# Optimization experiments

Hardware: AMD Instinct MI355X
Metric: run time of the kernel (lower is better)

Reference implementation:

```python
import jax, jax.numpy as jnp
import numpy as np

N, E, F, H = 100000, 1000000, 128, 64
BN_EPS = 1e-3  # keras BatchNormalization default epsilon


def setup_inputs() -> dict:
    key = jax.random.key(0)
    k_x, k_src, k_dst, k_w = jax.random.split(key, 4)
    node_features = jax.random.normal(k_x, (N, F), dtype=jnp.float32)
    # Ensure every node appears at least once as a source so that
    # deg**-0.5 is finite (the original code implicitly assumes this).
    src = jnp.concatenate([
        jnp.arange(N, dtype=jnp.int32),
        jax.random.randint(k_src, (E - N,), 0, N, dtype=jnp.int32),
    ])
    dst = jax.random.randint(k_dst, (E,), 0, N, dtype=jnp.int32)
    edge_index = jnp.stack([src, dst], axis=1)  # [E, 2]
    # glorot_uniform for kernel
    limit = np.sqrt(6.0 / (F + H)).astype(np.float32)
    W = jax.random.uniform(k_w, (F, H), dtype=jnp.float32, minval=-limit, maxval=limit)
    b = jnp.zeros((H,), dtype=jnp.float32)
    bn_gamma = jnp.ones((H,), dtype=jnp.float32)
    bn_beta = jnp.zeros((H,), dtype=jnp.float32)
    bn_mean = jnp.zeros((H,), dtype=jnp.float32)
    bn_var = jnp.ones((H,), dtype=jnp.float32)
    return dict(node_features=node_features, W=W, b=b, bn_gamma=bn_gamma,
                bn_beta=bn_beta, bn_mean=bn_mean, bn_var=bn_var,
                edge_index=edge_index)


def reference(node_features, W, b, bn_gamma, bn_beta, bn_mean, bn_var, edge_index):
    n = node_features.shape[0]
    src = edge_index[:, 0]
    dst = edge_index[:, 1]
    # Dense transform; dropout is identity in inference (training=False).
    h = node_features @ W + b  # [N, H]
    # Out-degree per node (segments keyed by src, matching the TF code).
    deg = jax.ops.segment_sum(jnp.ones(src.shape, h.dtype), src, num_segments=n)  # [N]
    inv_sqrt_deg = deg ** -0.5
    # Per-edge symmetric-style scaling: deg(src)^-0.5 * deg(dst)^-0.5 * h[dst]
    edge_scale = inv_sqrt_deg[src] * inv_sqrt_deg[dst]  # [E]
    neigh = edge_scale[:, None] * h[dst]  # [E, H]
    agg = 0.5 * jax.ops.segment_sum(neigh, src, num_segments=n)  # [N, H]
    # Self term: segment_mean of deg(src) * h[src] over src segments.
    self_term = deg[src][:, None] * h[src]  # [E, H]
    self_sum = jax.ops.segment_sum(self_term, src, num_segments=n)  # [N, H]
    self_mean = self_sum / jnp.maximum(deg, 1.0)[:, None]
    agg = agg + 0.5 * self_mean
    # BatchNormalization in inference mode.
    out = (agg - bn_mean) * (bn_gamma * jax.lax.rsqrt(bn_var + BN_EPS)) + bn_beta
    return out
```

## Files before the change

kernel.cpp:

```cpp
#include <hip/hip_runtime.h>

#define BN_EPS 0.001f
#define CAP 32

typedef __attribute__((ext_vector_type(8))) short bf16x8;
typedef __attribute__((ext_vector_type(4))) float f32x4;

__device__ __forceinline__ unsigned short f2bf(float f) {
  unsigned u = __float_as_uint(f);
  u += 0x7fffu + ((u >> 16) & 1u);
  return (unsigned short)(u >> 16);
}
__device__ __forceinline__ unsigned scale2(unsigned u, float s) {
  float lo = __uint_as_float(u << 16) * s;
  float hi = __uint_as_float(u & 0xffff0000u) * s;
  return (((unsigned)f2bf(hi)) << 16) | (unsigned)f2bf(lo);
}

__global__ __launch_bounds__(256) void k_fused(
    const float* __restrict__ X, const float* __restrict__ W,
    const float* __restrict__ B, unsigned short* __restrict__ hb, int N, int Gg,
    const int2* __restrict__ ei, int* __restrict__ cnt,
    int* __restrict__ ell_t, int E, int Gs) {
  __shared__ float WtF[4096];

  int g = blockIdx.x / 7;
  int r = blockIdx.x % 7;
  int tid = threadIdx.x;

  if (r >= 2) {
    int chunk = g * 5 + (r - 2);
    if (chunk >= Gs) return;
    int e = chunk * 256 + tid;
    if (e < E) {
      int2 sd = ei[e];
      int pos = atomicAdd(&cnt[sd.x], 1);
      if (pos < CAP) ell_t[(size_t)pos * N + sd.x] = sd.y;
    }
    return;
  }

  int tile = g * 2 + r;
  if (tile >= Gg) return;

  char* Wt = (char*)WtF;
  const float4* W4 = (const float4*)W;
  for (int i = tid; i < 2048; i += 256) {
    float4 v = W4[i];
    int k = i >> 4;
    int col0 = (i & 15) << 2;
    int kb2 = k << 1;
    *(unsigned short*)(Wt + (((col0 + 0) << 8) | (kb2 ^ (((col0 + 0) & 7) << 4)))) = f2bf(v.x);
    *(unsigned short*)(Wt + (((col0 + 1) << 8) | (kb2 ^ (((col0 + 1) & 7) << 4)))) = f2bf(v.y);
    *(unsigned short*)(Wt + (((col0 + 2) << 8) | (kb2 ^ (((col0 + 2) & 7) << 4)))) = f2bf(v.z);
    *(unsigned short*)(Wt + (((col0 + 3) << 8) | (kb2 ^ (((col0 + 3) & 7) << 4)))) = f2bf(v.w);
  }
  __syncthreads();

  int lane = tid & 63;
  int w = tid >> 6;
  int l15 = lane & 15;
  int lk = lane >> 4;

  int row0 = tile * 64;
  int rA = row0 + w * 16 + l15;
  bool rowok = rA < N;
  const float* xp = X + (size_t)rA * 128 + (lk << 3);

  f32x4 acc[4];
  #pragma unroll
  for (int n = 0; n < 4; ++n) {
    float bv = B[(n << 4) + l15];
    acc[n] = (f32x4){bv, bv, bv, bv};
  }

  #pragma unroll
  for (int kb = 0; kb < 4; ++kb) {
    bf16x8 af = {0, 0, 0, 0, 0, 0, 0, 0};
    if (rowok) {
      float4 x0 = *(const float4*)(xp + kb * 32);
      float4 x1 = *(const float4*)(xp + kb * 32 + 4);
      af[0] = (short)f2bf(x0.x); af[1] = (short)f2bf(x0.y);
      af[2] = (short)f2bf(x0.z); af[3] = (short)f2bf(x0.w);
      af[4] = (short)f2bf(x1.x); af[5] = (short)f2bf(x1.y);
      af[6] = (short)f2bf(x1.z); af[7] = (short)f2bf(x1.w);
    }
    int kbyte = (kb << 6) | (lk << 4);
    #pragma unroll
    for (int n = 0; n < 4; ++n) {
      int col = (n << 4) + l15;
      bf16x8 bfr = *(const bf16x8*)(Wt + ((col << 8) | (kbyte ^ ((col & 7) << 4))));
      acc[n] = __builtin_amdgcn_mfma_f32_16x16x32_bf16(af, bfr, acc[n], 0, 0, 0);
    }
  }

  int rbase = row0 + w * 16 + (lk << 2);
  #pragma unroll
  for (int n = 0; n < 4; ++n) {
    #pragma unroll
    for (int q = 0; q < 4; ++q) {
      int row = rbase + q;
      if (row < N) hb[(size_t)row * 64 + (n << 4) + l15] = f2bf(acc[n][q]);
    }
  }
}

__global__ __launch_bounds__(256) void k_scale(const unsigned int* __restrict__ hb32,
                                               const int* __restrict__ cnt,
                                               unsigned int* __restrict__ hbs32, int N) {
  int t = blockIdx.x * 256 + threadIdx.x;
  int node = t >> 3;
  int q = t & 7;
  if (node >= N) return;
  int c = cnt[node];
  float s = rsqrtf((float)((c > 0) ? c : 1));
  uint4 v = ((const uint4*)(hb32 + (size_t)node * 32))[q];
  v.x = scale2(v.x, s); v.y = scale2(v.y, s);
  v.z = scale2(v.z, s); v.w = scale2(v.w, s);
  ((uint4*)(hbs32 + (size_t)node * 32))[q] = v;
}

__global__ __launch_bounds__(256) void k_agg2(const int* __restrict__ cnt,
                                              const int* __restrict__ ell_t,
                                              const unsigned int* __restrict__ hb32,
                                              const unsigned int* __restrict__ hbs32,
                                              const float* __restrict__ gamma,
                                              const float* __restrict__ beta,
                                              const float* __restrict__ mean,
                                              const float* __restrict__ var,
                                              float* __restrict__ out, int N) {
  __shared__ int lds_dst[CAP * 64];
  __shared__ int lds_cnt[64];

  int tid = threadIdx.x;
  int node0 = blockIdx.x * 64;

  if (tid < 64) {
    int n = node0 + tid;
    lds_cnt[tid] = (n < N) ? cnt[n] : 0;
  }
  for (int i = tid; i < CAP * 64; i += 256) {
    int j = i & 63;
    int p = i >> 6;
    int n = node0 + j;
    lds_dst[i] = (n < N) ? ell_t[(size_t)p * N + n] : 0;
  }
  __syncthreads();

  int hw = tid >> 5;
  int fp = tid & 31;

  float2 gm = *(const float2*)&gamma[fp * 2];
  float2 bt = *(const float2*)&beta[fp * 2];
  float2 mn = *(const float2*)&mean[fp * 2];
  float2 vr = *(const float2*)&var[fp * 2];
  float gsx = gm.x * rsqrtf(vr.x + BN_EPS);
  float gsy = gm.y * rsqrtf(vr.y + BN_EPS);

  #pragma unroll
  for (int t = 0; t < 8; ++t) {
    int j = hw * 8 + t;
    int node = node0 + j;
    if (node >= N) continue;
    int c0 = lds_cnt[j];
    int c = (c0 < CAP) ? c0 : CAP;
    unsigned us = hb32[(size_t)node * 32 + fp];

    float ax = 0.f, ay = 0.f;
    int q = 0;
    for (; q + 8 <= c; q += 8) {
      int d[8];
      #pragma unroll
      for (int i = 0; i < 8; ++i) {
        int dr = lds_dst[(q + i) * 64 + j];
        d[i] = ((unsigned)dr < (unsigned)N) ? dr : 0;
      }
      unsigned u[8];
      #pragma unroll
      for (int i = 0; i < 8; ++i) u[i] = hbs32[(size_t)d[i] * 32 + fp];
      #pragma unroll
      for (int i = 0; i < 8; ++i) {
        ax += __uint_as_float(u[i] << 16);
        ay += __uint_as_float(u[i] & 0xffff0000u);
      }
    }
    if (q + 4 <= c) {
      int d0 = lds_dst[(q + 0) * 64 + j]; d0 = ((unsigned)d0 < (unsigned)N) ? d0 : 0;
      int d1 = lds_dst[(q + 1) * 64 + j]; d1 = ((unsigned)d1 < (unsigned)N) ? d1 : 0;
      int d2 = lds_dst[(q + 2) * 64 + j]; d2 = ((unsigned)d2 < (unsigned)N) ? d2 : 0;
      int d3 = lds_dst[(q + 3) * 64 + j]; d3 = ((unsigned)d3 < (unsigned)N) ? d3 : 0;
      unsigned u0 = hbs32[(size_t)d0 * 32 + fp];
      unsigned u1 = hbs32[(size_t)d1 * 32 + fp];
      unsigned u2 = hbs32[(size_t)d2 * 32 + fp];
      unsigned u3 = hbs32[(size_t)d3 * 32 + fp];
      ax += __uint_as_float(u0 << 16);
      ay += __uint_as_float(u0 & 0xffff0000u);
      ax += __uint_as_float(u1 << 16);
      ay += __uint_as_float(u1 & 0xffff0000u);
      ax += __uint_as_float(u2 << 16);
      ay += __uint_as_float(u2 & 0xffff0000u);
      ax += __uint_as_float(u3 << 16);
      ay += __uint_as_float(u3 & 0xffff0000u);
      q += 4;
    }
    for (; q < c; ++q) {
      int dq = lds_dst[q * 64 + j];
      dq = ((unsigned)dq < (unsigned)N) ? dq : 0;
      unsigned u = hbs32[(size_t)dq * 32 + fp];
      ax += __uint_as_float(u << 16);
      ay += __uint_as_float(u & 0xffff0000u);
    }

    float hx = __uint_as_float(us << 16);
    float hy = __uint_as_float(us & 0xffff0000u);
    float degf = (float)c0;
    float isd_n = rsqrtf((float)((c0 > 0) ? c0 : 1));
    float rx = 0.5f * (isd_n * ax + degf * hx);
    float ry = 0.5f * (isd_n * ay + degf * hy);

    float2 o;
    o.x = (rx - mn.x) * gsx + bt.x;
    o.y = (ry - mn.y) * gsy + bt.y;
    *(float2*)&out[(size_t)node * 64 + fp * 2] = o;
  }
}

__global__ __launch_bounds__(256) void k_agg2_g(const int* __restrict__ cnt,
                                                const int* __restrict__ ell_t,
                                                const unsigned int* __restrict__ hb32,
                                                const float* __restrict__ gamma,
                                                const float* __restrict__ beta,
                                                const float* __restrict__ mean,
                                                const float* __restrict__ var,
                                                float* __restrict__ out, int N) {
  __shared__ int lds_dst[CAP * 64];
  __shared__ int lds_cnt[64];

  int tid = threadIdx.x;
  int node0 = blockIdx.x * 64;

  if (tid < 64) {
    int n = node0 + tid;
    lds_cnt[tid] = (n < N) ? cnt[n] : 0;
  }
  for (int i = tid; i < CAP * 64; i += 256) {
    int j = i & 63;
    int p = i >> 6;
    int n = node0 + j;
    lds_dst[i] = (n < N) ? ell_t[(size_t)p * N + n] : 0;
  }
  __syncthreads();

  int hw = tid >> 5;
  int fp = tid & 31;

  float2 gm = *(const float2*)&gamma[fp * 2];
  float2 bt = *(const float2*)&beta[fp * 2];
  float2 mn = *(const float2*)&mean[fp * 2];
  float2 vr = *(const float2*)&var[fp * 2];
  float gsx = gm.x * rsqrtf(vr.x + BN_EPS);
  float gsy = gm.y * rsqrtf(vr.y + BN_EPS);

  for (int t = 0; t < 8; ++t) {
    int j = hw * 8 + t;
    int node = node0 + j;
    if (node >= N) continue;
    int c0 = lds_cnt[j];
    int c = (c0 < CAP) ? c0 : CAP;
    unsigned us = hb32[(size_t)node * 32 + fp];

    float ax = 0.f, ay = 0.f;
    int q = 0;
    for (; q + 4 <= c; q += 4) {
      int d0 = lds_dst[(q + 0) * 64 + j]; d0 = ((unsigned)d0 < (unsigned)N) ? d0 : 0;
      int d1 = lds_dst[(q + 1) * 64 + j]; d1 = ((unsigned)d1 < (unsigned)N) ? d1 : 0;
      int d2 = lds_dst[(q + 2) * 64 + j]; d2 = ((unsigned)d2 < (unsigned)N) ? d2 : 0;
      int d3 = lds_dst[(q + 3) * 64 + j]; d3 = ((unsigned)d3 < (unsigned)N) ? d3 : 0;
      float s0 = rsqrtf((float)max(cnt[d0], 1));
      float s1 = rsqrtf((float)max(cnt[d1], 1));
      float s2 = rsqrtf((float)max(cnt[d2], 1));
      float s3 = rsqrtf((float)max(cnt[d3], 1));
      unsigned u0 = hb32[(size_t)d0 * 32 + fp];
      unsigned u1 = hb32[(size_t)d1 * 32 + fp];
      unsigned u2 = hb32[(size_t)d2 * 32 + fp];
      unsigned u3 = hb32[(size_t)d3 * 32 + fp];
      ax = fmaf(s0, __uint_as_float(u0 << 16), ax);
      ay = fmaf(s0, __uint_as_float(u0 & 0xffff0000u), ay);
      ax = fmaf(s1, __uint_as_float(u1 << 16), ax);
      ay = fmaf(s1, __uint_as_float(u1 & 0xffff0000u), ay);
      ax = fmaf(s2, __uint_as_float(u2 << 16), ax);
      ay = fmaf(s2, __uint_as_float(u2 & 0xffff0000u), ay);
      ax = fmaf(s3, __uint_as_float(u3 << 16), ax);
      ay = fmaf(s3, __uint_as_float(u3 & 0xffff0000u), ay);
    }
    for (; q < c; ++q) {
      int dq = lds_dst[q * 64 + j];
      dq = ((unsigned)dq < (unsigned)N) ? dq : 0;
      float sq = rsqrtf((float)max(cnt[dq], 1));
      unsigned u = hb32[(size_t)dq * 32 + fp];
      ax = fmaf(sq, __uint_as_float(u << 16), ax);
      ay = fmaf(sq, __uint_as_float(u & 0xffff0000u), ay);
    }

    float hx = __uint_as_float(us << 16);
    float hy = __uint_as_float(us & 0xffff0000u);
    float degf = (float)c0;
    float isd_n = rsqrtf((float)((c0 > 0) ? c0 : 1));
    float rx = 0.5f * (isd_n * ax + degf * hx);
    float ry = 0.5f * (isd_n * ay + degf * hy);

    float2 o;
    o.x = (rx - mn.x) * gsx + bt.x;
    o.y = (ry - mn.y) * gsy + bt.y;
    *(float2*)&out[(size_t)node * 64 + fp * 2] = o;
  }
}

extern "C" void kernel_launch(void* const* d_in, const int* in_sizes, int n_in,
                              void* d_out, int out_size, void* d_ws, size_t ws_size,
                              hipStream_t stream) {
  const float* X     = (const float*)d_in[0];
  const float* W     = (const float*)d_in[1];
  const float* B     = (const float*)d_in[2];
  const float* gamma = (const float*)d_in[3];
  const float* beta  = (const float*)d_in[4];
  const float* mean  = (const float*)d_in[5];
  const float* var   = (const float*)d_in[6];
  const int2*  ei    = (const int2*)d_in[7];

  int N = in_sizes[0] / 128;
  int E = in_sizes[7] / 2;
  float* out = (float*)d_out;

  size_t hb_elems = (size_t)N * 64;
  size_t need_hbs = hb_elems * 2 * 2 + (size_t)N * CAP * 4 + (size_t)N * 4;

  int Gs = (E + 255) / 256;
  int Gg = (N + 63) / 64;
  int g7 = (Gg + 1) / 2;
  int g5 = (Gs + 4) / 5;
  int groups = (g7 > g5) ? g7 : g5;
  int Ga = (N + 63) / 64;

  if (ws_size >= need_hbs) {
    unsigned short* hb  = (unsigned short*)d_ws;
    unsigned short* hbs = hb + hb_elems;
    int*            ell = (int*)(hbs + hb_elems);
    int*            cnt = ell + (size_t)N * CAP;

    hipMemsetAsync(cnt, 0, (size_t)N * sizeof(int), stream);
    k_fused<<<groups * 7, 256, 0, stream>>>(X, W, B, hb, N, Gg, ei, cnt, ell, E, Gs);
    k_scale<<<(N * 8 + 255) / 256, 256, 0, stream>>>((const unsigned int*)hb, cnt,
                                                     (unsigned int*)hbs, N);
    k_agg2<<<Ga, 256, 0, stream>>>(cnt, ell, (const unsigned int*)hb,
                                   (const unsigned int*)hbs,
                                   gamma, beta, mean, var, out, N);
  } else {
    unsigned short* hb  = (unsigned short*)d_ws;
    int*            ell = (int*)(hb + hb_elems);
    int*            cnt = ell + (size_t)N * CAP;

    hipMemsetAsync(cnt, 0, (size_t)N * sizeof(int), stream);
    k_fused<<<groups * 7, 256, 0, stream>>>(X, W, B, hb, N, Gg, ei, cnt, ell, E, Gs);
    k_agg2_g<<<Ga, 256, 0, stream>>>(cnt, ell, (const unsigned int*)hb,
                                     gamma, beta, mean, var, out, N);
  }
}
```

Baseline: 199.5 us.

## Fuse all stages into one persistent cooperative kernel with grid syncs

Replaces the memset plus three kernel launches with a single cooperative persistent kernel that zeroes counts, runs the GEMM and the ELL build, scales h, and aggregates, separated by grid-wide syncs. The aim is to remove launch gaps and the per-launch tail effects between the small stages. In exchange it limits the grid to resident blocks, loops over tiles, and adds grid-barrier cost plus the W-to-LDS conversion once per block. It also drops the 4-wide remainder block in the old k_agg2 fallback.

```diff
diff --git a/kernel.cpp b/kernel.cpp
--- a/kernel.cpp
+++ b/kernel.cpp
@@ -1,4 +1,7 @@
 #include <hip/hip_runtime.h>
+#include <hip/hip_cooperative_groups.h>
+
+namespace cg = cooperative_groups;
 
 #define BN_EPS 0.001f
 #define CAP 32
@@ -15,6 +18,259 @@
   float lo = __uint_as_float(u << 16) * s;
   float hi = __uint_as_float(u & 0xffff0000u) * s;
   return (((unsigned)f2bf(hi)) << 16) | (unsigned)f2bf(lo);
+}
+
+__global__ __launch_bounds__(256, 4) void k_all(
+    const float* __restrict__ X, const float* __restrict__ W,
+    const float* __restrict__ B, const float* __restrict__ gamma,
+    const float* __restrict__ beta, const float* __restrict__ mean,
+    const float* __restrict__ var, const int2* __restrict__ ei,
+    unsigned short* __restrict__ hb, unsigned short* __restrict__ hbs,
+    int* __restrict__ ell_t, int* __restrict__ cnt,
+    float* __restrict__ out, int N, int E, int use_hbs) {
+  __shared__ float WtF[4096];
+  cg::grid_group gg = cg::this_grid();
+  int tid = threadIdx.x;
+  int bid = blockIdx.x;
+  int nb  = gridDim.x;
+
+  for (int i = bid * 256 + tid; i < N; i += nb * 256) cnt[i] = 0;
+  gg.sync();
+
+  char* Wt = (char*)WtF;
+  {
+    const float4* W4 = (const float4*)W;
+    for (int i = tid; i < 2048; i += 256) {
+      float4 v = W4[i];
+      int k = i >> 4;
+      int col0 = (i & 15) << 2;
+      int kb2 = k << 1;
+      *(unsigned short*)(Wt + (((col0 + 0) << 8) | (kb2 ^ (((col0 + 0) & 7) << 4)))) = f2bf(v.x);
+      *(unsigned short*)(Wt + (((col0 + 1) << 8) | (kb2 ^ (((col0 + 1) & 7) << 4)))) = f2bf(v.y);
+      *(unsigned short*)(Wt + (((col0 + 2) << 8) | (kb2 ^ (((col0 + 2) & 7) << 4)))) = f2bf(v.z);
+      *(unsigned short*)(Wt + (((col0 + 3) << 8) | (kb2 ^ (((col0 + 3) & 7) << 4)))) = f2bf(v.w);
+    }
+  }
+  __syncthreads();
+
+  int Gg = (N + 63) >> 6;
+  int Gs = (E + 255) >> 8;
+  int g7 = (Gg + 1) >> 1;
+  int g5 = (Gs + 4) / 5;
+  int groups = (g7 > g5) ? g7 : g5;
+  int total = groups * 7;
+
+  int lane = tid & 63;
+  int w = tid >> 6;
+  int l15 = lane & 15;
+  int lk = lane >> 4;
+
+  for (int u = bid; u < total; u += nb) {
+    int g = u / 7, r = u % 7;
+    if (r >= 2) {
+      int chunk = g * 5 + (r - 2);
+      if (chunk < Gs) {
+        int e = chunk * 256 + tid;
+        if (e < E) {
+          int2 sd = ei[e];
+          int pos = atomicAdd(&cnt[sd.x], 1);
+          if (pos < CAP) ell_t[(size_t)pos * N + sd.x] = sd.y;
+        }
+      }
+    } else {
+      int tile = g * 2 + r;
+      if (tile < Gg) {
+        int row0 = tile * 64;
+        int rA = row0 + w * 16 + l15;
+        bool rowok = rA < N;
+        const float* xp = X + (size_t)rA * 128 + (lk << 3);
+
+        f32x4 acc[4];
+        #pragma unroll
+        for (int n = 0; n < 4; ++n) {
+          float bv = B[(n << 4) + l15];
+          acc[n] = (f32x4){bv, bv, bv, bv};
+        }
+        #pragma unroll
+        for (int kb = 0; kb < 4; ++kb) {
+          bf16x8 af = {0, 0, 0, 0, 0, 0, 0, 0};
+          if (rowok) {
+            float4 x0 = *(const float4*)(xp + kb * 32);
+            float4 x1 = *(const float4*)(xp + kb * 32 + 4);
+            af[0] = (short)f2bf(x0.x); af[1] = (short)f2bf(x0.y);
+            af[2] = (short)f2bf(x0.z); af[3] = (short)f2bf(x0.w);
+            af[4] = (short)f2bf(x1.x); af[5] = (short)f2bf(x1.y);
+            af[6] = (short)f2bf(x1.z); af[7] = (short)f2bf(x1.w);
+          }
+          int kbyte = (kb << 6) | (lk << 4);
+          #pragma unroll
+          for (int n = 0; n < 4; ++n) {
+            int col = (n << 4) + l15;
+            bf16x8 bfr = *(const bf16x8*)(Wt + ((col << 8) | (kbyte ^ ((col & 7) << 4))));
+            acc[n] = __builtin_amdgcn_mfma_f32_16x16x32_bf16(af, bfr, acc[n], 0, 0, 0);
+          }
+        }
+        int rbase = row0 + w * 16 + (lk << 2);
+        #pragma unroll
+        for (int n = 0; n < 4; ++n) {
+          #pragma unroll
+          for (int q = 0; q < 4; ++q) {
+            int row = rbase + q;
+            if (row < N) hb[(size_t)row * 64 + (n << 4) + l15] = f2bf(acc[n][q]);
+          }
+        }
+      }
+    }
+  }
+  __threadfence();
+  gg.sync();
+
+  if (use_hbs) {
+    const unsigned* hb32r = (const unsigned*)hb;
+    unsigned* hbs32w = (unsigned*)hbs;
+    int tot = N * 8;
+    for (int t = bid * 256 + tid; t < tot; t += nb * 256) {
+      int node = t >> 3;
+      int q = t & 7;
+      int c = cnt[node];
+      float s = rsqrtf((float)((c > 0) ? c : 1));
+      uint4 v = ((const uint4*)(hb32r + (size_t)node * 32))[q];
+      v.x = scale2(v.x, s); v.y = scale2(v.y, s);
+      v.z = scale2(v.z, s); v.w = scale2(v.w, s);
+      ((uint4*)(hbs32w + (size_t)node * 32))[q] = v;
+    }
+  }
+  __threadfence();
+  gg.sync();
+
+  int* lds_dst = (int*)WtF;
+  int* lds_cnt = ((int*)WtF) + CAP * 64;
+  const unsigned* hb32 = (const unsigned*)hb;
+  const unsigned* hbs32 = (const unsigned*)hbs;
+  int hw = tid >> 5;
+  int fp = tid & 31;
+
+  float2 gm = *(const float2*)&gamma[fp * 2];
+  float2 bt = *(const float2*)&beta[fp * 2];
+  float2 mn = *(const float2*)&mean[fp * 2];
+  float2 vr = *(const float2*)&var[fp * 2];
+  float gsx = gm.x * rsqrtf(vr.x + BN_EPS);
+  float gsy = gm.y * rsqrtf(vr.y + BN_EPS);
+
+  int Ga = (N + 63) >> 6;
+  for (int tile = bid; tile < Ga; tile += nb) {
+    int node0 = tile << 6;
+    if (tid < 64) {
+      int n = node0 + tid;
+      lds_cnt[tid] = (n < N) ? cnt[n] : 0;
+    }
+    for (int i = tid; i < CAP * 64; i += 256) {
+      int j = i & 63;
+      int p = i >> 6;
+      int n = node0 + j;
+      lds_dst[i] = (n < N) ? ell_t[(size_t)p * N + n] : 0;
+    }
+    __syncthreads();
+
+    #pragma unroll 2
+    for (int t = 0; t < 8; ++t) {
+      int j = hw * 8 + t;
+      int node = node0 + j;
+      if (node < N) {
+        int c0 = lds_cnt[j];
+        int c = (c0 < CAP) ? c0 : CAP;
+        unsigned us = hb32[(size_t)node * 32 + fp];
+
+        float ax = 0.f, ay = 0.f;
+        if (use_hbs) {
+          int q = 0;
+          for (; q + 8 <= c; q += 8) {
+            int d[8];
+            #pragma unroll
+            for (int i = 0; i < 8; ++i) {
+              int dr = lds_dst[(q + i) * 64 + j];
+              d[i] = ((unsigned)dr < (unsigned)N) ? dr : 0;
+            }
+            unsigned u[8];
+            #pragma unroll
+            for (int i = 0; i < 8; ++i) u[i] = hbs32[(size_t)d[i] * 32 + fp];
+            #pragma unroll
+            for (int i = 0; i < 8; ++i) {
+              ax += __uint_as_float(u[i] << 16);
+              ay += __uint_as_float(u[i] & 0xffff0000u);
+            }
+          }
+          if (q + 4 <= c) {
+            int d0 = lds_dst[(q + 0) * 64 + j]; d0 = ((unsigned)d0 < (unsigned)N) ? d0 : 0;
+            int d1 = lds_dst[(q + 1) * 64 + j]; d1 = ((unsigned)d1 < (unsigned)N) ? d1 : 0;
+            int d2 = lds_dst[(q + 2) * 64 + j]; d2 = ((unsigned)d2 < (unsigned)N) ? d2 : 0;
+            int d3 = lds_dst[(q + 3) * 64 + j]; d3 = ((unsigned)d3 < (unsigned)N) ? d3 : 0;
+            unsigned u0 = hbs32[(size_t)d0 * 32 + fp];
+            unsigned u1 = hbs32[(size_t)d1 * 32 + fp];
+            unsigned u2 = hbs32[(size_t)d2 * 32 + fp];
+            unsigned u3 = hbs32[(size_t)d3 * 32 + fp];
+            ax += __uint_as_float(u0 << 16); ay += __uint_as_float(u0 & 0xffff0000u);
+            ax += __uint_as_float(u1 << 16); ay += __uint_as_float(u1 & 0xffff0000u);
+            ax += __uint_as_float(u2 << 16); ay += __uint_as_float(u2 & 0xffff0000u);
+            ax += __uint_as_float(u3 << 16); ay += __uint_as_float(u3 & 0xffff0000u);
+            q += 4;
+          }
+          for (; q < c; ++q) {
+            int dq = lds_dst[q * 64 + j];
+            dq = ((unsigned)dq < (unsigned)N) ? dq : 0;
+            unsigned u = hbs32[(size_t)dq * 32 + fp];
+            ax += __uint_as_float(u << 16);
+            ay += __uint_as_float(u & 0xffff0000u);
+          }
+        } else {
+          int q = 0;
+          for (; q + 4 <= c; q += 4) {
+            int d0 = lds_dst[(q + 0) * 64 + j]; d0 = ((unsigned)d0 < (unsigned)N) ? d0 : 0;
+            int d1 = lds_dst[(q + 1) * 64 + j]; d1 = ((unsigned)d1 < (unsigned)N) ? d1 : 0;
+            int d2 = lds_dst[(q + 2) * 64 + j]; d2 = ((unsigned)d2 < (unsigned)N) ? d2 : 0;
+            int d3 = lds_dst[(q + 3) * 64 + j]; d3 = ((unsigned)d3 < (unsigned)N) ? d3 : 0;
+            float s0 = rsqrtf((float)max(cnt[d0], 1));
+            float s1 = rsqrtf((float)max(cnt[d1], 1));
+            float s2 = rsqrtf((float)max(cnt[d2], 1));
+            float s3 = rsqrtf((float)max(cnt[d3], 1));
+            unsigned u0 = hb32[(size_t)d0 * 32 + fp];
+            unsigned u1 = hb32[(size_t)d1 * 32 + fp];
+            unsigned u2 = hb32[(size_t)d2 * 32 + fp];
+            unsigned u3 = hb32[(size_t)d3 * 32 + fp];
+            ax = fmaf(s0, __uint_as_float(u0 << 16), ax);
+            ay = fmaf(s0, __uint_as_float(u0 & 0xffff0000u), ay);
+            ax = fmaf(s1, __uint_as_float(u1 << 16), ax);
+            ay = fmaf(s1, __uint_as_float(u1 & 0xffff0000u), ay);
+            ax = fmaf(s2, __uint_as_float(u2 << 16), ax);
+            ay = fmaf(s2, __uint_as_float(u2 & 0xffff0000u), ay);
+            ax = fmaf(s3, __uint_as_float(u3 << 16), ax);
+            ay = fmaf(s3, __uint_as_float(u3 & 0xffff0000u), ay);
+          }
+          for (; q < c; ++q) {
+            int dq = lds_dst[q * 64 + j];
+            dq = ((unsigned)dq < (unsigned)N) ? dq : 0;
+            float sq = rsqrtf((float)max(cnt[dq], 1));
+            unsigned u = hb32[(size_t)dq * 32 + fp];
+            ax = fmaf(sq, __uint_as_float(u << 16), ax);
+            ay = fmaf(sq, __uint_as_float(u & 0xffff0000u), ay);
+          }
+        }
+
+        float hx = __uint_as_float(us << 16);
+        float hy = __uint_as_float(us & 0xffff0000u);
+        float degf = (float)c0;
+        float isd_n = rsqrtf((float)((c0 > 0) ? c0 : 1));
+        float rx = 0.5f * (isd_n * ax + degf * hx);
+        float ry = 0.5f * (isd_n * ay + degf * hy);
+
+        float2 o;
+        o.x = (rx - mn.x) * gsx + bt.x;
+        o.y = (ry - mn.y) * gsy + bt.y;
+        *(float2*)&out[(size_t)node * 64 + fp * 2] = o;
+      }
+    }
+    __syncthreads();
+  }
 }
 
 __global__ __launch_bounds__(256) void k_fused(
@@ -23,7 +279,6 @@
     const int2* __restrict__ ei, int* __restrict__ cnt,
     int* __restrict__ ell_t, int E, int Gs) {
   __shared__ float WtF[4096];
-
   int g = blockIdx.x / 7;
   int r = blockIdx.x % 7;
   int tid = threadIdx.x;
@@ -73,7 +328,6 @@
     float bv = B[(n << 4) + l15];
     acc[n] = (f32x4){bv, bv, bv, bv};
   }
-
   #pragma unroll
   for (int kb = 0; kb < 4; ++kb) {
     bf16x8 af = {0, 0, 0, 0, 0, 0, 0, 0};
@@ -93,7 +347,6 @@
       acc[n] = __builtin_amdgcn_mfma_f32_16x16x32_bf16(af, bfr, acc[n], 0, 0, 0);
     }
   }
-
   int rbase = row0 + w * 16 + (lk << 2);
   #pragma unroll
   for (int n = 0; n < 4; ++n) {
@@ -131,7 +384,6 @@
                                               float* __restrict__ out, int N) {
   __shared__ int lds_dst[CAP * 64];
   __shared__ int lds_cnt[64];
-
   int tid = threadIdx.x;
   int node0 = blockIdx.x * 64;
 
@@ -149,7 +401,6 @@
 
   int hw = tid >> 5;
   int fp = tid & 31;
-
   float2 gm = *(const float2*)&gamma[fp * 2];
   float2 bt = *(const float2*)&beta[fp * 2];
   float2 mn = *(const float2*)&mean[fp * 2];
@@ -184,25 +435,6 @@
         ay += __uint_as_float(u[i] & 0xffff0000u);
       }
     }
-    if (q + 4 <= c) {
-      int d0 = lds_dst[(q + 0) * 64 + j]; d0 = ((unsigned)d0 < (unsigned)N) ? d0 : 0;
-      int d1 = lds_dst[(q + 1) * 64 + j]; d1 = ((unsigned)d1 < (unsigned)N) ? d1 : 0;
-      int d2 = lds_dst[(q + 2) * 64 + j]; d2 = ((unsigned)d2 < (unsigned)N) ? d2 : 0;
-      int d3 = lds_dst[(q + 3) * 64 + j]; d3 = ((unsigned)d3 < (unsigned)N) ? d3 : 0;
-      unsigned u0 = hbs32[(size_t)d0 * 32 + fp];
-      unsigned u1 = hbs32[(size_t)d1 * 32 + fp];
-      unsigned u2 = hbs32[(size_t)d2 * 32 + fp];
-      unsigned u3 = hbs32[(size_t)d3 * 32 + fp];
-      ax += __uint_as_float(u0 << 16);
-      ay += __uint_as_float(u0 & 0xffff0000u);
-      ax += __uint_as_float(u1 << 16);
-      ay += __uint_as_float(u1 & 0xffff0000u);
-      ax += __uint_as_float(u2 << 16);
-      ay += __uint_as_float(u2 & 0xffff0000u);
-      ax += __uint_as_float(u3 << 16);
-      ay += __uint_as_float(u3 & 0xffff0000u);
-      q += 4;
-    }
     for (; q < c; ++q) {
       int dq = lds_dst[q * 64 + j];
       dq = ((unsigned)dq < (unsigned)N) ? dq : 0;
@@ -235,7 +467,6 @@
                                                 float* __restrict__ out, int N) {
   __shared__ int lds_dst[CAP * 64];
   __shared__ int lds_cnt[64];
-
   int tid = threadIdx.x;
   int node0 = blockIdx.x * 64;
 
@@ -253,7 +484,6 @@
 
   int hw = tid >> 5;
   int fp = tid & 31;
-
   float2 gm = *(const float2*)&gamma[fp * 2];
   float2 bt = *(const float2*)&beta[fp * 2];
   float2 mn = *(const float2*)&mean[fp * 2];
@@ -332,9 +562,49 @@
   int E = in_sizes[7] / 2;
   float* out = (float*)d_out;
 
-  size_t hb_elems = (size_t)N * 64;
-  size_t need_hbs = hb_elems * 2 * 2 + (size_t)N * CAP * 4 + (size_t)N * 4;
-
+  size_t hb_bytes = (size_t)N * 64 * 2;
+  size_t need_hbs = hb_bytes * 2 + (size_t)N * CAP * 4 + (size_t)N * 4;
+  int use_hbs = (ws_size >= need_hbs) ? 1 : 0;
+
+  unsigned short* hb;
+  unsigned short* hbs;
+  int* ell;
+  int* cnt;
+  if (use_hbs) {
+    hb  = (unsigned short*)d_ws;
+    hbs = hb + (size_t)N * 64;
+    ell = (int*)(hbs + (size_t)N * 64);
+    cnt = ell + (size_t)N * CAP;
+  } else {
+    hb  = (unsigned short*)d_ws;
+    hbs = hb;
+    ell = (int*)(hb + (size_t)N * 64);
+    cnt = ell + (size_t)N * CAP;
+  }
+
+  static int s_grid = 0;
+  if (s_grid == 0) {
+    int dev = 0;
+    hipGetDevice(&dev);
+    int cus = 0;
+    hipDeviceGetAttribute(&cus, hipDeviceAttributeMultiprocessorCount, dev);
+    if (cus <= 0) cus = 256;
+    int maxb = 0;
+    hipOccupancyMaxActiveBlocksPerMultiprocessor(&maxb, k_all, 256, 0);
+    if (maxb <= 0) maxb = 1;
+    s_grid = cus * maxb;
+    if (s_grid > 4096) s_grid = 4096;
+  }
+
+  void* args[] = {(void*)&X, (void*)&W, (void*)&B, (void*)&gamma, (void*)&beta,
+                  (void*)&mean, (void*)&var, (void*)&ei, (void*)&hb, (void*)&hbs,
+                  (void*)&ell, (void*)&cnt, (void*)&out, (void*)&N, (void*)&E,
+                  (void*)&use_hbs};
+  hipError_t err = hipLaunchCooperativeKernel((const void*)k_all, dim3(s_grid),
+                                              dim3(256), args, 0, stream);
+  if (err == hipSuccess) return;
+
+  hipMemsetAsync(cnt, 0, (size_t)N * sizeof(int), stream);
   int Gs = (E + 255) / 256;
   int Gg = (N + 63) / 64;
   int g7 = (Gg + 1) / 2;
@@ -342,26 +612,14 @@
   int groups = (g7 > g5) ? g7 : g5;
   int Ga = (N + 63) / 64;
 
-  if (ws_size >= need_hbs) {
-    unsigned short* hb  = (unsigned short*)d_ws;
-    unsigned short* hbs = hb + hb_elems;
-    int*            ell = (int*)(hbs + hb_elems);
-    int*            cnt = ell + (size_t)N * CAP;
-
-    hipMemsetAsync(cnt, 0, (size_t)N * sizeof(int), stream);
-    k_fused<<<groups * 7, 256, 0, stream>>>(X, W, B, hb, N, Gg, ei, cnt, ell, E, Gs);
+  k_fused<<<groups * 7, 256, 0, stream>>>(X, W, B, hb, N, Gg, ei, cnt, ell, E, Gs);
+  if (use_hbs) {
     k_scale<<<(N * 8 + 255) / 256, 256, 0, stream>>>((const unsigned int*)hb, cnt,
                                                      (unsigned int*)hbs, N);
     k_agg2<<<Ga, 256, 0, stream>>>(cnt, ell, (const unsigned int*)hb,
                                    (const unsigned int*)hbs,
                                    gamma, beta, mean, var, out, N);
   } else {
-    unsigned short* hb  = (unsigned short*)d_ws;
-    int*            ell = (int*)(hb + hb_elems);
-    int*            cnt = ell + (size_t)N * CAP;
-
-    hipMemsetAsync(cnt, 0, (size_t)N * sizeof(int), stream);
-    k_fused<<<groups * 7, 256, 0, stream>>>(X, W, B, hb, N, Gg, ei, cnt, ell, E, Gs);
     k_agg2_g<<<Ga, 256, 0, stream>>>(cnt, ell, (const unsigned int*)hb,
                                      gamma, beta, mean, var, out, N);
   }
```

Result: slower. 693.8 us (+247.8%).

## Partition edge scatter by source-node range to localize atomics and ELL writes

Applied to the files above, without the earlier changes.

The ELL-build blocks now each take a 2048-edge segment and one of 8 source-node partitions. A block processes only the edges whose source falls in its partition, so the atomic counter updates and scattered ELL stores from a block land in a narrower address range, with the aim of better cache locality. The cost is that every edge is read 8 times, and the number of scatter blocks grows, which changes how they interleave with the GEMM tiles in the fused launch. The remaining edit only reformats the aggregation loop.

```diff
diff --git a/kernel.cpp b/kernel.cpp
--- a/kernel.cpp
+++ b/kernel.cpp
@@ -2,6 +2,8 @@
 
 #define BN_EPS 0.001f
 #define CAP 32
+#define NPART 8
+#define SEGE 2048
 
 typedef __attribute__((ext_vector_type(8))) short bf16x8;
 typedef __attribute__((ext_vector_type(4))) float f32x4;
@@ -29,13 +31,23 @@
   int tid = threadIdx.x;
 
   if (r >= 2) {
-    int chunk = g * 5 + (r - 2);
-    if (chunk >= Gs) return;
-    int e = chunk * 256 + tid;
-    if (e < E) {
-      int2 sd = ei[e];
-      int pos = atomicAdd(&cnt[sd.x], 1);
-      if (pos < CAP) ell_t[(size_t)pos * N + sd.x] = sd.y;
+    int u = g * 5 + (r - 2);
+    if (u >= Gs) return;
+    int p   = u & (NPART - 1);
+    int seg = u >> 3;
+    int lo = (int)((size_t)p * N / NPART);
+    int hi = (int)((size_t)(p + 1) * N / NPART);
+    int base = seg * SEGE;
+    #pragma unroll
+    for (int i = 0; i < 8; ++i) {
+      int e = base + i * 256 + tid;
+      if (e < E) {
+        int2 sd = ei[e];
+        if (sd.x >= lo && sd.x < hi) {
+          int pos = atomicAdd(&cnt[sd.x], 1);
+          if (pos < CAP) ell_t[(size_t)pos * N + sd.x] = sd.y;
+        }
+      }
     }
     return;
   }
@@ -193,14 +205,10 @@
       unsigned u1 = hbs32[(size_t)d1 * 32 + fp];
       unsigned u2 = hbs32[(size_t)d2 * 32 + fp];
       unsigned u3 = hbs32[(size_t)d3 * 32 + fp];
-      ax += __uint_as_float(u0 << 16);
-      ay += __uint_as_float(u0 & 0xffff0000u);
-      ax += __uint_as_float(u1 << 16);
-      ay += __uint_as_float(u1 & 0xffff0000u);
-      ax += __uint_as_float(u2 << 16);
-      ay += __uint_as_float(u2 & 0xffff0000u);
-      ax += __uint_as_float(u3 << 16);
-      ay += __uint_as_float(u3 & 0xffff0000u);
+      ax += __uint_as_float(u0 << 16); ay += __uint_as_float(u0 & 0xffff0000u);
+      ax += __uint_as_float(u1 << 16); ay += __uint_as_float(u1 & 0xffff0000u);
+      ax += __uint_as_float(u2 << 16); ay += __uint_as_float(u2 & 0xffff0000u);
+      ax += __uint_as_float(u3 << 16); ay += __uint_as_float(u3 & 0xffff0000u);
       q += 4;
     }
     for (; q < c; ++q) {
@@ -335,7 +343,7 @@
   size_t hb_elems = (size_t)N * 64;
   size_t need_hbs = hb_elems * 2 * 2 + (size_t)N * CAP * 4 + (size_t)N * 4;
 
-  int Gs = (E + 255) / 256;
+  int Gs = NPART * ((E + SEGE - 1) / SEGE);
   int Gg = (N + 63) / 64;
   int g7 = (Gg + 1) / 2;
   int g5 = (Gs + 4) / 5;
```

Measured after the change: 179.3 us. 1.11x faster.
